# Kernel optimization log

Measured on AMD Instinct MI355X. Metric: run time of the kernel, lower is better.

Reference implementation:

```python
import jax, jax.numpy as jnp
import numpy as np

B, N, C = 4, 2048, 768
H = 12
D = C // H  # 64

def setup_inputs() -> dict:
    key = jax.random.key(0)
    k1, k2, k3 = jax.random.split(key, 3)
    x = jax.random.normal(k1, (B, N, C), dtype=jnp.float32)
    qkv_w = jax.random.normal(k2, (3 * C, C), dtype=jnp.float32) * (C ** -0.5)
    proj_w = jax.random.normal(k3, (C, C), dtype=jnp.float32) * (C ** -0.5)
    return {"x": x, "qkv_w": qkv_w, "proj_w": proj_w}

def reference(x, qkv_w, proj_w):
    b, n, c = x.shape
    h, d = H, c // H
    # qkv projection (Linear, no bias): [B,N,3C] -> [3,B,H,N,D]
    qkv = jnp.einsum('bnc,fc->bnf', x, qkv_w)
    qkv = qkv.reshape(b, n, 3, h, d).transpose(2, 0, 3, 1, 4)
    q, k, v = qkv[0], qkv[1], qkv[2]
    # scaled dot-product attention; module divides by sqrt(head_dim)
    scale = 1.0 / jnp.sqrt(jnp.float32(d)).astype(x.dtype)
    score = jnp.einsum('bhqd,bhkd->bhqk', q, k) * scale  # [B,H,N,N] full matrix, as in source
    attn = jax.nn.softmax(score, axis=-1)
    ctx = jnp.einsum('bhqk,bhkd->bhqd', attn, v)
    ctx = ctx.transpose(0, 2, 1, 3).reshape(b, n, c)
    out = jnp.einsum('bnc,oc->bno', ctx, proj_w)  # proj Linear, no bias; dropout p=0
    return out
```

## Files before the change

kernel.cpp:

```cpp
#include <hip/hip_runtime.h>
#include <hip/hip_bf16.h>

#define BB 4
#define NN 2048
#define CC 768
#define HH 12
#define DD 64
#define MTOT (BB*NN)

typedef __attribute__((ext_vector_type(8))) short frag16;
typedef __attribute__((ext_vector_type(4))) float f32x4;
typedef __attribute__((ext_vector_type(16))) float f32x16;
typedef __attribute__((ext_vector_type(4))) unsigned int u32x4;

static __device__ __forceinline__ float bf2f(unsigned short u) {
  unsigned int x = ((unsigned int)u) << 16;
  return __builtin_bit_cast(float, x);
}
static __device__ __forceinline__ unsigned short f2bf(float f) {
  __hip_bfloat16 h = __float2bfloat16(f);
  return __builtin_bit_cast(unsigned short, h);
}
static __device__ __forceinline__ unsigned int cvt_pk_bf16(float lo, float hi) {
  unsigned int r;
  asm("v_cvt_pk_bf16_f32 %0, %1, %2" : "=v"(r) : "v"(lo), "v"(hi));
  return r;
}
static __device__ __forceinline__ void gload16(const void* g, void* l) {
  __builtin_amdgcn_global_load_lds((const __attribute__((address_space(1))) void*)g,
                                   (__attribute__((address_space(3))) void*)l, 16, 0, 0);
}

#define QSCALE 0.18033688011112042f

__global__ void detect_k(const unsigned short* x, int* flag) {
  __shared__ int cnt;
  if (threadIdx.x == 0) cnt = 0;
  __syncthreads();
  float v = bf2f(x[threadIdx.x]);
  float a = fabsf(v);
  int weird = (!(a <= 1e4f)) || (a != 0.0f && a < 1e-10f);
  if (weird) atomicAdd(&cnt, 1);
  __syncthreads();
  if (threadIdx.x == 0) *flag = (cnt >= 24) ? 1 : 0;
}

__global__ void conv_k(const void* __restrict__ src, unsigned short* __restrict__ dst,
                       int n, const int* __restrict__ flag) {
  int fp32 = *flag;
  int i0 = (blockIdx.x * blockDim.x + threadIdx.x) * 4;
  int stride = gridDim.x * blockDim.x * 4;
  if (fp32) {
    const float* s = (const float*)src;
    for (int i = i0; i < n; i += stride) {
      float4 v = *reinterpret_cast<const float4*>(&s[i]);
      ushort4 o;
      o.x = f2bf(v.x); o.y = f2bf(v.y); o.z = f2bf(v.z); o.w = f2bf(v.w);
      *reinterpret_cast<ushort4*>(&dst[i]) = o;
    }
  } else {
    const unsigned short* s = (const unsigned short*)src;
    for (int i = i0; i < n; i += stride)
      *reinterpret_cast<ushort4*>(&dst[i]) = *reinterpret_cast<const ushort4*>(&s[i]);
  }
}

template<int EPI>
__global__ __launch_bounds__(256) void gemm_bt(const unsigned short* __restrict__ A,
                                               const unsigned short* __restrict__ Bw,
                                               unsigned short* __restrict__ qkvbuf,
                                               void* __restrict__ outp,
                                               const int* __restrict__ flag) {
  constexpr int K = CC;
  __shared__ unsigned short Asm[128 * 32];
  __shared__ unsigned short Bsm[128 * 32];
  const int tid = threadIdx.x;
  const int lane = tid & 63;
  const int w = tid >> 6;
  const int wm = w >> 1, wn = w & 1;
  const int l15 = lane & 15;
  const int g = lane >> 4;
  const int m0 = blockIdx.x * 128;
  const int f0 = blockIdx.y * 128;

  f32x4 acc[4][4];
#pragma unroll
  for (int i = 0; i < 4; ++i)
#pragma unroll
    for (int j = 0; j < 4; ++j) acc[i][j] = (f32x4){0.f, 0.f, 0.f, 0.f};

  const unsigned short* Abase = A + (size_t)m0 * K;
  const unsigned short* Bbase = Bw + (size_t)f0 * K;

  for (int kt = 0; kt < K / 32; ++kt) {
    const int k0 = kt * 32;
    __syncthreads();
#pragma unroll
    for (int i = 0; i < 2; ++i) {
      int chunk = (i * 4 + w) * 64 + lane;
      int row = chunk >> 2;
      int col = (chunk & 3) << 3;
      gload16(Abase + (size_t)row * K + k0 + col, (char*)Asm + (i * 4 + w) * 1024);
      gload16(Bbase + (size_t)row * K + k0 + col, (char*)Bsm + (i * 4 + w) * 1024);
    }
    __syncthreads();

    frag16 af[4], bfv[4];
#pragma unroll
    for (int t = 0; t < 4; ++t) {
      af[t]  = *reinterpret_cast<const frag16*>(&Asm[(wm * 64 + t * 16 + l15) * 32 + 8 * g]);
      bfv[t] = *reinterpret_cast<const frag16*>(&Bsm[(wn * 64 + t * 16 + l15) * 32 + 8 * g]);
    }
    __builtin_amdgcn_s_setprio(1);
#pragma unroll
    for (int i = 0; i < 4; ++i)
#pragma unroll
      for (int j = 0; j < 4; ++j)
        acc[i][j] = __builtin_amdgcn_mfma_f32_16x16x32_bf16(af[i], bfv[j], acc[i][j], 0, 0, 0);
    __builtin_amdgcn_s_setprio(0);
  }

  if constexpr (EPI == 0) {
    const size_t plane = (size_t)BB * HH * NN * DD;
#pragma unroll
    for (int i = 0; i < 4; ++i) {
      int mbase = m0 + wm * 64 + i * 16 + 4 * g;
#pragma unroll
      for (int j = 0; j < 4; ++j) {
        int f = f0 + wn * 64 + j * 16 + l15;
        int which = f / CC;
        int rem = f - which * CC;
        int h = rem >> 6, d = rem & 63;
        if (which == 2) {
          int b = mbase >> 11, n = mbase & 2047;
          int nsw = (n & ~63) | ((n & 63) ^ ((d & 7) << 3));
          ushort4 o;
#pragma unroll
          for (int r = 0; r < 4; ++r) ((unsigned short*)&o)[r] = f2bf(acc[i][j][r]);
          size_t idx = 2 * plane + (((size_t)(b * HH + h) * DD + d) * NN + nsw);
          *reinterpret_cast<ushort4*>(&qkvbuf[idx]) = o;
        } else if (which == 1) {
#pragma unroll
          for (int r = 0; r < 4; ++r) {
            int mm = mbase + r;
            int b = mm >> 11, n = mm & 2047;
            int dsw = d ^ ((n & 7) << 3);
            size_t idx = plane + (((size_t)(b * HH + h) * NN + n) * DD + dsw);
            qkvbuf[idx] = f2bf(acc[i][j][r]);
          }
        } else {
#pragma unroll
          for (int r = 0; r < 4; ++r) {
            int mm = mbase + r;
            int b = mm >> 11, n = mm & 2047;
            size_t idx = (((size_t)(b * HH + h) * NN + n) * DD + d);
            qkvbuf[idx] = f2bf(acc[i][j][r] * QSCALE);
          }
        }
      }
    }
  } else {
    int fp32 = *flag;
#pragma unroll
    for (int i = 0; i < 4; ++i) {
      int mbase = m0 + wm * 64 + i * 16 + 4 * g;
#pragma unroll
      for (int j = 0; j < 4; ++j) {
        int f = f0 + wn * 64 + j * 16 + l15;
#pragma unroll
        for (int r = 0; r < 4; ++r) {
          size_t idx = (size_t)(mbase + r) * CC + f;
          if (fp32) ((float*)outp)[idx] = acc[i][j][r];
          else ((unsigned short*)outp)[idx] = f2bf(acc[i][j][r]);
        }
      }
    }
  }
}

template<int SPLIT>
__global__ __launch_bounds__(512) void attn_k(const unsigned short* __restrict__ qkv,
                                              unsigned short* __restrict__ outp,
                                              float* __restrict__ ml) {
  __shared__ unsigned short Kb[2][64 * 64];
  __shared__ unsigned short Vb[2][64 * 64];
  const int tid = threadIdx.x;
  const int lane = tid & 63;
  const int w = tid >> 6;
  const int l31 = lane & 31;
  const int hl = lane >> 5;

  int orig = blockIdx.x;
  int sp, bh, q0, kvbeg, kvend;
  if constexpr (SPLIT) {
    int wgid = (orig & 7) * 96 + (orig >> 3);
    sp = wgid / 384;
    int rem = wgid - sp * 384;
    bh = rem >> 3;
    q0 = (rem & 7) * 256;
    kvbeg = sp * 16;
    kvend = kvbeg + 16;
  } else {
    int wgid = (orig & 7) * 48 + (orig >> 3);
    sp = 0;
    bh = wgid >> 3;
    q0 = (wgid & 7) * 256;
    kvbeg = 0;
    kvend = NN / 64;
  }

  const size_t plane = (size_t)BB * HH * NN * DD;
  const unsigned short* Qg = qkv + (size_t)bh * NN * DD;
  const unsigned short* Kg = qkv + plane + (size_t)bh * NN * DD;
  const unsigned short* Vt = qkv + 2 * plane + (size_t)bh * NN * DD;

  frag16 qb[4];
  {
    int qrow = q0 + w * 32 + l31;
#pragma unroll
    for (int s = 0; s < 4; ++s)
      qb[s] = *reinterpret_cast<const frag16*>(&Qg[(size_t)qrow * DD + s * 16 + hl * 8]);
  }

  f32x16 acc0, acc1;
#pragma unroll
  for (int i = 0; i < 16; ++i) { acc0[i] = 0.f; acc1[i] = 0.f; }
  float lsum = 0.f;

  const int srow = tid >> 3;
  const int scol = (tid & 7) * 8;
#define STAGE(buf, n0)                                                   \
  {                                                                      \
    gload16(Kg + (size_t)((n0) + srow) * DD + scol, &Kb[buf][tid * 8]);  \
    gload16(Vt + (size_t)srow * NN + (n0) + scol, &Vb[buf][tid * 8]);    \
  }

  int cur = 0;
  STAGE(0, kvbeg * 64)

  for (int kv = kvbeg; kv < kvend; ++kv) {
    __syncthreads();
    if (kv + 1 < kvend) STAGE(cur ^ 1, (kv + 1) * 64)

    const char* Kc = (const char*)&Kb[cur][0];
    const char* Vc = (const char*)&Vb[cur][0];
    const int xk = (l31 & 7) << 4;

    f32x16 s0, s1;
#pragma unroll
    for (int i = 0; i < 16; ++i) { s0[i] = 0.f; s1[i] = 0.f; }
    __builtin_amdgcn_s_setprio(1);
#pragma unroll
    for (int s = 0; s < 4; ++s) {
      frag16 ka = *reinterpret_cast<const frag16*>(
          Kc + (l31) * 128 + (((s * 16 + hl * 8) * 2) ^ xk));
      s0 = __builtin_amdgcn_mfma_f32_32x32x16_bf16(ka, qb[s], s0, 0, 0, 0);
    }
#pragma unroll
    for (int s = 0; s < 4; ++s) {
      frag16 ka = *reinterpret_cast<const frag16*>(
          Kc + (32 + l31) * 128 + (((s * 16 + hl * 8) * 2) ^ xk));
      s1 = __builtin_amdgcn_mfma_f32_32x32x16_bf16(ka, qb[s], s1, 0, 0, 0);
    }
    __builtin_amdgcn_s_setprio(0);

#pragma unroll
    for (int r = 0; r < 16; ++r) s0[r] = __builtin_amdgcn_exp2f(s0[r]);
#pragma unroll
    for (int r = 0; r < 16; ++r) s1[r] = __builtin_amdgcn_exp2f(s1[r]);
    {
      float a0 = s0[0] + s1[0], a1 = s0[1] + s1[1], a2 = s0[2] + s1[2], a3 = s0[3] + s1[3];
#pragma unroll
      for (int r = 4; r < 16; r += 4) {
        a0 += s0[r] + s1[r];
        a1 += s0[r + 1] + s1[r + 1];
        a2 += s0[r + 2] + s1[r + 2];
        a3 += s0[r + 3] + s1[r + 3];
      }
      float tot = (a0 + a1) + (a2 + a3);
      tot += __shfl_xor(tot, 32);
      lsum += tot;
    }

    frag16 pA0, pA1, pB0, pB1;
    {
      unsigned int wv[8], xw[8];
#pragma unroll
      for (int i = 0; i < 8; ++i) wv[i] = cvt_pk_bf16(s0[2 * i], s0[2 * i + 1]);
#pragma unroll
      for (int i = 0; i < 8; ++i) xw[i] = (unsigned int)__shfl_xor((int)wv[i], 32);
      u32x4 f0v = {hl ? xw[2] : wv[0], hl ? xw[3] : wv[1], hl ? wv[2] : xw[0], hl ? wv[3] : xw[1]};
      u32x4 f1v = {hl ? xw[6] : wv[4], hl ? xw[7] : wv[5], hl ? wv[6] : xw[4], hl ? wv[7] : xw[5]};
      pA0 = __builtin_bit_cast(frag16, f0v);
      pA1 = __builtin_bit_cast(frag16, f1v);
    }
    {
      unsigned int wv[8], xw[8];
#pragma unroll
      for (int i = 0; i < 8; ++i) wv[i] = cvt_pk_bf16(s1[2 * i], s1[2 * i + 1]);
#pragma unroll
      for (int i = 0; i < 8; ++i) xw[i] = (unsigned int)__shfl_xor((int)wv[i], 32);
      u32x4 f0v = {hl ? xw[2] : wv[0], hl ? xw[3] : wv[1], hl ? wv[2] : xw[0], hl ? wv[3] : xw[1]};
      u32x4 f1v = {hl ? xw[6] : wv[4], hl ? xw[7] : wv[5], hl ? wv[6] : xw[4], hl ? wv[7] : xw[5]};
      pB0 = __builtin_bit_cast(frag16, f0v);
      pB1 = __builtin_bit_cast(frag16, f1v);
    }

    __builtin_amdgcn_s_setprio(1);
#pragma unroll
    for (int dh = 0; dh < 2; ++dh) {
      f32x16& a = dh ? acc1 : acc0;
      frag16 vb;
      vb = *reinterpret_cast<const frag16*>(
          Vc + (dh * 32 + l31) * 128 + (((hl * 8) * 2) ^ xk));
      a = __builtin_amdgcn_mfma_f32_32x32x16_bf16(pA0, vb, a, 0, 0, 0);
      vb = *reinterpret_cast<const frag16*>(
          Vc + (dh * 32 + l31) * 128 + (((16 + hl * 8) * 2) ^ xk));
      a = __builtin_amdgcn_mfma_f32_32x32x16_bf16(pA1, vb, a, 0, 0, 0);
      vb = *reinterpret_cast<const frag16*>(
          Vc + (dh * 32 + l31) * 128 + (((32 + hl * 8) * 2) ^ xk));
      a = __builtin_amdgcn_mfma_f32_32x32x16_bf16(pB0, vb, a, 0, 0, 0);
      vb = *reinterpret_cast<const frag16*>(
          Vc + (dh * 32 + l31) * 128 + (((32 + 16 + hl * 8) * 2) ^ xk));
      a = __builtin_amdgcn_mfma_f32_32x32x16_bf16(pB1, vb, a, 0, 0, 0);
    }
    __builtin_amdgcn_s_setprio(0);
    cur ^= 1;
  }

  float inv = 1.0f / lsum;
  if constexpr (SPLIT) {
    size_t rowbase = ((size_t)(sp * (BB * HH) + bh) * NN + q0 + w * 32);
#pragma unroll
    for (int r = 0; r < 16; ++r) {
      int qr = (r & 3) + 8 * (r >> 2) + 4 * hl;
      float ivr = __shfl(inv, qr);
      size_t base = (rowbase + qr) * DD;
      outp[base + l31] = f2bf(acc0[r] * ivr);
      outp[base + 32 + l31] = f2bf(acc1[r] * ivr);
    }
    if (hl == 0) {
      size_t mlrow = (size_t)sp * (BB * HH * NN) + (size_t)bh * NN + q0 + w * 32 + l31;
      ml[mlrow] = lsum;
    }
  } else {
    const int b = bh / HH, h = bh - b * HH;
#pragma unroll
    for (int r = 0; r < 16; ++r) {
      int qr = (r & 3) + 8 * (r >> 2) + 4 * hl;
      float ivr = __shfl(inv, qr);
      int qn = q0 + w * 32 + qr;
      size_t base = ((size_t)(b * NN + qn)) * CC + h * DD;
      outp[base + l31] = f2bf(acc0[r] * ivr);
      outp[base + 32 + l31] = f2bf(acc1[r] * ivr);
    }
  }
#undef STAGE
}

__global__ __launch_bounds__(256) void combine_k(const unsigned short* __restrict__ ctxp,
                                                 const float* __restrict__ ml,
                                                 unsigned short* __restrict__ ctx) {
  const int tid = threadIdx.x;
  const int row = blockIdx.x * 32 + (tid >> 3);
  const int d0 = (tid & 7) * 8;
  const size_t PL = (size_t)BB * HH * NN * DD;
  const size_t MLP = (size_t)BB * HH * NN;
  float l0 = ml[row], l1 = ml[MLP + row];
  float inv = 1.0f / (l0 + l1);
  float w0 = l0 * inv, w1 = l1 * inv;
  u32x4 a = *reinterpret_cast<const u32x4*>(&ctxp[(size_t)row * DD + d0]);
  u32x4 bq = *reinterpret_cast<const u32x4*>(&ctxp[PL + (size_t)row * DD + d0]);
  const unsigned short* ap = (const unsigned short*)&a;
  const unsigned short* bp = (const unsigned short*)&bq;
  ushort4 o[2];
#pragma unroll
  for (int j = 0; j < 8; ++j)
    ((unsigned short*)o)[j] = f2bf(w0 * bf2f(ap[j]) + w1 * bf2f(bp[j]));
  const int bh = row >> 11, q = row & 2047;
  const int b = bh / HH, h = bh - b * HH;
  size_t base = ((size_t)(b * NN + q)) * CC + h * DD + d0;
  *reinterpret_cast<u32x4*>(&ctx[base]) = *reinterpret_cast<u32x4*>(&o[0]);
}

extern "C" void kernel_launch(void* const* d_in, const int* in_sizes, int n_in,
                              void* d_out, int out_size, void* d_ws, size_t ws_size,
                              hipStream_t stream) {
  const void* x = d_in[0];
  const void* qw = d_in[1];
  const void* pw = d_in[2];
  char* ws = (char*)d_ws;
  int* flag = (int*)ws;
  size_t off = 256;
  unsigned short* xb = (unsigned short*)(ws + off); off += (size_t)MTOT * CC * 2;
  unsigned short* qwb = (unsigned short*)(ws + off); off += (size_t)3 * CC * CC * 2;
  unsigned short* pwb = (unsigned short*)(ws + off); off += (size_t)CC * CC * 2;
  unsigned short* qkvbuf = (unsigned short*)(ws + off); off += (size_t)3 * MTOT * CC * 2;
  unsigned short* ctxp = (unsigned short*)(ws + off);
  size_t off2 = off + (size_t)2 * BB * HH * NN * DD * 2;
  float* ml = (float*)(ws + off2);
  size_t need = off2 + (size_t)2 * BB * HH * NN * 4;
  unsigned short* ctx = xb;

  detect_k<<<1, 256, 0, stream>>>((const unsigned short*)x, flag);
  conv_k<<<1024, 256, 0, stream>>>(x, xb, MTOT * CC, flag);
  conv_k<<<512, 256, 0, stream>>>(qw, qwb, 3 * CC * CC, flag);
  conv_k<<<256, 256, 0, stream>>>(pw, pwb, CC * CC, flag);
  gemm_bt<0><<<dim3(MTOT / 128, (3 * CC) / 128), 256, 0, stream>>>(xb, qwb, qkvbuf, nullptr, flag);
  if (ws_size >= need) {
    attn_k<1><<<768, 512, 0, stream>>>(qkvbuf, ctxp, ml);
    combine_k<<<3072, 256, 0, stream>>>(ctxp, ml, ctx);
  } else {
    attn_k<0><<<384, 512, 0, stream>>>(qkvbuf, ctx, nullptr);
  }
  gemm_bt<1><<<dim3(MTOT / 128, CC / 128), 256, 0, stream>>>(ctx, pwb, nullptr, d_out, flag);
}
```

Measured before the change: 170.7 us.

## Double-buffer GEMM shared tiles and skip the copy pass for bf16 inputs

The GEMM kernel now uses two shared-memory buffers and issues the next K-tile's global-to-LDS loads before computing on the current tile. This cuts the syncthreads per iteration from two to one and overlaps load latency with MFMA work. The conversion kernels now return early when inputs are already bf16, and the GEMM reads the raw input pointers directly in that case, which removes a copy pass. With fp32 inputs (the default here), conversion still runs, so the gain should come mainly from the pipelining, at the cost of doubled LDS use per block.

Result: faster. 158.1 us (-7.4%).

```diff
diff --git a/kernel.cpp b/kernel.cpp
--- a/kernel.cpp
+++ b/kernel.cpp
@@ -47,33 +47,29 @@
 
 __global__ void conv_k(const void* __restrict__ src, unsigned short* __restrict__ dst,
                        int n, const int* __restrict__ flag) {
-  int fp32 = *flag;
+  if (!*flag) return;
+  const float* s = (const float*)src;
   int i0 = (blockIdx.x * blockDim.x + threadIdx.x) * 4;
   int stride = gridDim.x * blockDim.x * 4;
-  if (fp32) {
-    const float* s = (const float*)src;
-    for (int i = i0; i < n; i += stride) {
-      float4 v = *reinterpret_cast<const float4*>(&s[i]);
-      ushort4 o;
-      o.x = f2bf(v.x); o.y = f2bf(v.y); o.z = f2bf(v.z); o.w = f2bf(v.w);
-      *reinterpret_cast<ushort4*>(&dst[i]) = o;
-    }
-  } else {
-    const unsigned short* s = (const unsigned short*)src;
-    for (int i = i0; i < n; i += stride)
-      *reinterpret_cast<ushort4*>(&dst[i]) = *reinterpret_cast<const ushort4*>(&s[i]);
+  for (int i = i0; i < n; i += stride) {
+    float4 v = *reinterpret_cast<const float4*>(&s[i]);
+    ushort4 o;
+    o.x = f2bf(v.x); o.y = f2bf(v.y); o.z = f2bf(v.z); o.w = f2bf(v.w);
+    *reinterpret_cast<ushort4*>(&dst[i]) = o;
   }
 }
 
 template<int EPI>
-__global__ __launch_bounds__(256) void gemm_bt(const unsigned short* __restrict__ A,
-                                               const unsigned short* __restrict__ Bw,
+__global__ __launch_bounds__(256) void gemm_bt(const unsigned short* __restrict__ Araw,
+                                               const unsigned short* __restrict__ Aconv,
+                                               const unsigned short* __restrict__ Braw,
+                                               const unsigned short* __restrict__ Bconv,
                                                unsigned short* __restrict__ qkvbuf,
                                                void* __restrict__ outp,
                                                const int* __restrict__ flag) {
   constexpr int K = CC;
-  __shared__ unsigned short Asm[128 * 32];
-  __shared__ unsigned short Bsm[128 * 32];
+  __shared__ unsigned short Asm[2][128 * 32];
+  __shared__ unsigned short Bsm[2][128 * 32];
   const int tid = threadIdx.x;
   const int lane = tid & 63;
   const int w = tid >> 6;
@@ -82,6 +78,10 @@
   const int g = lane >> 4;
   const int m0 = blockIdx.x * 128;
   const int f0 = blockIdx.y * 128;
+  const int fp32 = *flag;
+
+  const unsigned short* A = fp32 ? Aconv : Araw;
+  const unsigned short* Bw = fp32 ? Bconv : Braw;
 
   f32x4 acc[4][4];
 #pragma unroll
@@ -92,24 +92,32 @@
   const unsigned short* Abase = A + (size_t)m0 * K;
   const unsigned short* Bbase = Bw + (size_t)f0 * K;
 
+#define GSTAGE(buf, k0)                                                               \
+  {                                                                                   \
+    _Pragma("unroll")                                                                 \
+    for (int i_ = 0; i_ < 2; ++i_) {                                                  \
+      int chunk = (i_ * 4 + w) * 64 + lane;                                           \
+      int row = chunk >> 2;                                                           \
+      int col = (chunk & 3) << 3;                                                     \
+      gload16(Abase + (size_t)row * K + (k0) + col,                                   \
+              (char*)&Asm[buf][0] + (i_ * 4 + w) * 1024);                             \
+      gload16(Bbase + (size_t)row * K + (k0) + col,                                   \
+              (char*)&Bsm[buf][0] + (i_ * 4 + w) * 1024);                             \
+    }                                                                                 \
+  }
+
+  int cur = 0;
+  GSTAGE(0, 0)
+
   for (int kt = 0; kt < K / 32; ++kt) {
-    const int k0 = kt * 32;
     __syncthreads();
-#pragma unroll
-    for (int i = 0; i < 2; ++i) {
-      int chunk = (i * 4 + w) * 64 + lane;
-      int row = chunk >> 2;
-      int col = (chunk & 3) << 3;
-      gload16(Abase + (size_t)row * K + k0 + col, (char*)Asm + (i * 4 + w) * 1024);
-      gload16(Bbase + (size_t)row * K + k0 + col, (char*)Bsm + (i * 4 + w) * 1024);
-    }
-    __syncthreads();
+    if (kt + 1 < K / 32) GSTAGE(cur ^ 1, (kt + 1) * 32)
 
     frag16 af[4], bfv[4];
 #pragma unroll
     for (int t = 0; t < 4; ++t) {
-      af[t]  = *reinterpret_cast<const frag16*>(&Asm[(wm * 64 + t * 16 + l15) * 32 + 8 * g]);
-      bfv[t] = *reinterpret_cast<const frag16*>(&Bsm[(wn * 64 + t * 16 + l15) * 32 + 8 * g]);
+      af[t]  = *reinterpret_cast<const frag16*>(&Asm[cur][(wm * 64 + t * 16 + l15) * 32 + 8 * g]);
+      bfv[t] = *reinterpret_cast<const frag16*>(&Bsm[cur][(wn * 64 + t * 16 + l15) * 32 + 8 * g]);
     }
     __builtin_amdgcn_s_setprio(1);
 #pragma unroll
@@ -118,7 +126,9 @@
       for (int j = 0; j < 4; ++j)
         acc[i][j] = __builtin_amdgcn_mfma_f32_16x16x32_bf16(af[i], bfv[j], acc[i][j], 0, 0, 0);
     __builtin_amdgcn_s_setprio(0);
-  }
+    cur ^= 1;
+  }
+#undef GSTAGE
 
   if constexpr (EPI == 0) {
     const size_t plane = (size_t)BB * HH * NN * DD;
@@ -160,7 +170,7 @@
       }
     }
   } else {
-    int fp32 = *flag;
+    int ofp32 = fp32;
 #pragma unroll
     for (int i = 0; i < 4; ++i) {
       int mbase = m0 + wm * 64 + i * 16 + 4 * g;
@@ -170,7 +180,7 @@
 #pragma unroll
         for (int r = 0; r < 4; ++r) {
           size_t idx = (size_t)(mbase + r) * CC + f;
-          if (fp32) ((float*)outp)[idx] = acc[i][j][r];
+          if (ofp32) ((float*)outp)[idx] = acc[i][j][r];
           else ((unsigned short*)outp)[idx] = f2bf(acc[i][j][r]);
         }
       }
@@ -406,12 +416,14 @@
   conv_k<<<1024, 256, 0, stream>>>(x, xb, MTOT * CC, flag);
   conv_k<<<512, 256, 0, stream>>>(qw, qwb, 3 * CC * CC, flag);
   conv_k<<<256, 256, 0, stream>>>(pw, pwb, CC * CC, flag);
-  gemm_bt<0><<<dim3(MTOT / 128, (3 * CC) / 128), 256, 0, stream>>>(xb, qwb, qkvbuf, nullptr, flag);
+  gemm_bt<0><<<dim3(MTOT / 128, (3 * CC) / 128), 256, 0, stream>>>(
+      (const unsigned short*)x, xb, (const unsigned short*)qw, qwb, qkvbuf, nullptr, flag);
   if (ws_size >= need) {
     attn_k<1><<<768, 512, 0, stream>>>(qkvbuf, ctxp, ml);
     combine_k<<<3072, 256, 0, stream>>>(ctxp, ml, ctx);
   } else {
     attn_k<0><<<384, 512, 0, stream>>>(qkvbuf, ctx, nullptr);
   }
-  gemm_bt<1><<<dim3(MTOT / 128, CC / 128), 256, 0, stream>>>(ctx, pwb, nullptr, d_out, flag);
-}
+  gemm_bt<1><<<dim3(MTOT / 128, CC / 128), 256, 0, stream>>>(
+      ctx, ctx, (const unsigned short*)pw, pwb, nullptr, d_out, flag);
+}
```
